# Kernel tuning notes

Measured on AMD Instinct MI355X. Metric: run time of the kernel, lower is better.

The kernel has to match this reference:

```python
import jax, jax.numpy as jnp
import numpy as np

B, T, INP, E, H, N = 16, 256, 1536, 512, 8, 16
D = E // H            # 64, must equal default dim_head for to_out shapes to work
SCALE = D ** -0.5
EPS = 1e-5


def _ln(x, g, b):
    m = x.mean(-1, keepdims=True)
    v = ((x - m) ** 2).mean(-1, keepdims=True)
    return (x - m) * jax.lax.rsqrt(v + EPS) * g + b


def _attend(q, k, v, Wo, bo):
    # q,k,v: [bt, h, n, d]. NOTE: attend is LogSoftmax, not Softmax (faithful).
    dots = jnp.einsum('bhnd,bhmd->bhnm', q, k) * SCALE
    a = jax.nn.log_softmax(dots, axis=-1)
    o = jnp.einsum('bhnm,bhmd->bhnd', a, v)
    o = o.transpose(0, 2, 1, 3).reshape(o.shape[0], N, E)  # b n (h d)
    return o @ Wo + bo


def _self_attn(x, Wqkv, Wo, bo):
    # x is already LayerNormed (PreNorm); residual adds the normed x (faithful).
    qkv = x @ Wqkv  # [bt, n, 3E]
    q, k, v = jnp.split(qkv, 3, axis=-1)
    hd = lambda t: t.reshape(t.shape[0], N, H, D).transpose(0, 2, 1, 3)
    return _attend(hd(q), hd(k), hd(v), Wo, bo) + x


def _ff(x, W1, b1, W2, b2):
    # x already LayerNormed; residual adds normed x (faithful to PreNorm+FF).
    return jax.nn.gelu(x @ W1 + b1, approximate=False) @ W2 + b2 + x


def setup_inputs() -> dict:
    key = jax.random.key(0)
    ks = iter(jax.random.split(key, 64))
    nrm = lambda shape, s=0.02: jax.random.normal(next(ks), shape, jnp.float32) * s
    inp = {
        'features': jax.random.normal(next(ks), (B, T, INP), jnp.float32),
        'targets_array': jax.random.randint(next(ks), (B, T), 0, N, jnp.int64),
        'emb': nrm((N, E), 1.0),
        'Wf': nrm((INP, 2 * E * N)), 'bf': jnp.zeros((2 * E * N,), jnp.float32),
        # layer 0: Attention (tuple path: only to_out used)
        'att0_Wo': nrm((E, E)), 'att0_bo': jnp.zeros((E,), jnp.float32),
        'Wm': nrm((E, 1)), 'bm': jnp.zeros((1,), jnp.float32),
    }
    for i in range(3):
        inp[f'ff{i}_g'] = jnp.ones((E,), jnp.float32)
        inp[f'ff{i}_b'] = jnp.zeros((E,), jnp.float32)
        inp[f'ff{i}_W1'] = nrm((E, 2 * E)); inp[f'ff{i}_b1'] = jnp.zeros((2 * E,), jnp.float32)
        inp[f'ff{i}_W2'] = nrm((2 * E, E)); inp[f'ff{i}_b2'] = jnp.zeros((E,), jnp.float32)
    for i in (1, 2):
        inp[f'att{i}_g'] = jnp.ones((E,), jnp.float32)
        inp[f'att{i}_b'] = jnp.zeros((E,), jnp.float32)
        inp[f'att{i}_Wqkv'] = nrm((E, 3 * E))
        inp[f'att{i}_Wo'] = nrm((E, E)); inp[f'att{i}_bo'] = jnp.zeros((E,), jnp.float32)
    return inp


def reference(features, targets_array, emb, Wf, bf, att0_Wo, att0_bo, Wm, bm,
              ff0_g, ff0_b, ff0_W1, ff0_b1, ff0_W2, ff0_b2,
              ff1_g, ff1_b, ff1_W1, ff1_b1, ff1_W2, ff1_b2,
              ff2_g, ff2_b, ff2_W1, ff2_b1, ff2_W2, ff2_b2,
              att1_g, att1_b, att1_Wqkv, att1_Wo, att1_bo,
              att2_g, att2_b, att2_Wqkv, att2_Wo, att2_bo):
    f = features.reshape(-1, INP)                 # [BT, INP]
    t = targets_array.reshape(-1)                 # [BT]
    kv = f @ Wf + bf                              # [BT, 2*E*N]
    k_, v_ = jnp.split(kv, 2, axis=-1)
    nhd = lambda x: x.reshape(-1, N, H, D).transpose(0, 2, 1, 3)  # b (n h d) -> b h n d
    k, v = nhd(k_), nhd(v_)
    q = emb[t].reshape(-1, H, 1, D)               # b h d -> b h 1 d
    q = jnp.broadcast_to(q, (q.shape[0], H, N, D))
    # layer stack: Attn(tuple), PreNorm(FF), PreNorm(Attn), PreNorm(FF), PreNorm(Attn), PreNorm(FF)
    x = _attend(q, k, v, att0_Wo, att0_bo)        # [BT, N, E]
    x = _ff(_ln(x, ff0_g, ff0_b), ff0_W1, ff0_b1, ff0_W2, ff0_b2)
    x = _self_attn(_ln(x, att1_g, att1_b), att1_Wqkv, att1_Wo, att1_bo)
    x = _ff(_ln(x, ff1_g, ff1_b), ff1_W1, ff1_b1, ff1_W2, ff1_b2)
    x = _self_attn(_ln(x, att2_g, att2_b), att2_Wqkv, att2_Wo, att2_bo)
    x = _ff(_ln(x, ff2_g, ff2_b), ff2_W1, ff2_b1, ff2_W2, ff2_b2)
    out = x.mean(axis=1)                          # mean over targets -> [BT, E]
    out = out.reshape(B, T, E)
    mean = out @ Wm + bm                          # [B, T, 1]
    return mean
```

## Files before the change

kernel.cpp:

```cpp
#include <hip/hip_runtime.h>
#include <math.h>

#define BTOT 4096
#define INP  1536
#define EDIM 512
#define NTOK 16
#define KVW  16384
#define ENW  8192
#define FFH  1024
#define NDOT 2048

typedef __attribute__((ext_vector_type(8))) __bf16 bf16x8;
typedef __attribute__((ext_vector_type(4))) float f32x4;

__device__ __forceinline__ ushort f2bf(float f) {
    union { float f; unsigned u; } v; v.f = f;
    unsigned r = v.u + 0x7fffu + ((v.u >> 16) & 1u);
    return (ushort)(r >> 16);
}
__device__ __forceinline__ float bf2f(ushort h) {
    union { unsigned u; float f; } v; v.u = ((unsigned)h) << 16;
    return v.f;
}

__device__ __forceinline__ void transpose_body(
    const float* in, int ld, int c0, int R, ushort* out,
    int bx, int by, int tid)
{
    __shared__ float t[64][65];
    const int bc = bx * 64 + c0;
    const int br = by * 64;
#pragma unroll
    for (int it = 0; it < 16; ++it) {
        int idx = tid + it * 256;
        int r = idx >> 6, c = idx & 63;
        t[r][c] = in[(size_t)(br + r) * ld + bc + c];
    }
    __syncthreads();
    const int C0 = bx * 64;
#pragma unroll
    for (int it = 0; it < 4; ++it) {
        int idx = tid + it * 256;
        int cc = idx >> 4, rp = idx & 15;
        uint2 w2;
        w2.x = f2bf(t[4 * rp + 0][cc]) | ((unsigned)f2bf(t[4 * rp + 1][cc]) << 16);
        w2.y = f2bf(t[4 * rp + 2][cc]) | ((unsigned)f2bf(t[4 * rp + 3][cc]) << 16);
        *reinterpret_cast<uint2*>(out + (size_t)(C0 + cc) * R + br + 4 * rp) = w2;
    }
}

struct TJob { const float* in; ushort* out; int ld, c0, R, gbx, boffs; };
struct TJobs { TJob j[10]; };

__global__ __launch_bounds__(256) void transpose_all_k(TJobs jobs)
{
    const int b = blockIdx.x;
    int ji = 0;
    while (ji < 9 && b >= jobs.j[ji + 1].boffs) ++ji;
    TJob jb = jobs.j[ji];
    const int rel = b - jb.boffs;
    transpose_body(jb.in, jb.ld, jb.c0, jb.R, jb.out,
                   rel % jb.gbx, rel / jb.gbx, threadIdx.x);
}

__global__ __launch_bounds__(256) void conv_all_k(
    const float* __restrict__ features, ushort* __restrict__ featb,
    const float* __restrict__ wq0, const float* __restrict__ wq1,
    ushort* __restrict__ wv0, ushort* __restrict__ wv1)
{
    const int b = blockIdx.x;
    if (b < 3072) {
        const int i = b * 256 + threadIdx.x;
        const float4* p = reinterpret_cast<const float4*>(features) + 2 * (size_t)i;
        float4 a = p[0], c = p[1];
        uint4 o;
        o.x = f2bf(a.x) | ((unsigned)f2bf(a.y) << 16);
        o.y = f2bf(a.z) | ((unsigned)f2bf(a.w) << 16);
        o.z = f2bf(c.x) | ((unsigned)f2bf(c.y) << 16);
        o.w = f2bf(c.z) | ((unsigned)f2bf(c.w) << 16);
        reinterpret_cast<uint4*>(featb)[i] = o;
    } else {
        const int bb = b - 3072;
        const float* src = (bb >= 128) ? wq1 : wq0;
        ushort* dst = (bb >= 128) ? wv1 : wv0;
        const int idx = (bb & 127) * 256 + threadIdx.x;
        const int row = idx >> 6, c8 = (idx & 63) * 8;
        const float4* p = reinterpret_cast<const float4*>(
            src + (size_t)row * (3 * EDIM) + 2 * EDIM + c8);
        float4 a = p[0], c = p[1];
        uint4 o;
        o.x = f2bf(a.x) | ((unsigned)f2bf(a.y) << 16);
        o.y = f2bf(a.z) | ((unsigned)f2bf(a.w) << 16);
        o.z = f2bf(c.x) | ((unsigned)f2bf(c.y) << 16);
        o.w = f2bf(c.z) | ((unsigned)f2bf(c.w) << 16);
        *reinterpret_cast<uint4*>(dst + (size_t)row * EDIM + c8) = o;
    }
}

__global__ __launch_bounds__(256) void gproj_k(
    const float* __restrict__ Wf, const float* __restrict__ bfv,
    const float* __restrict__ emb, ushort* __restrict__ BTg,
    float* __restrict__ C0s, const int* __restrict__ targets,
    int* __restrict__ perm, int* __restrict__ boff)
{
    if (blockIdx.y == 8) {
        if (blockIdx.x != 0) return;
        __shared__ int cnt[NTOK], off_s[NTOK], cur[NTOK];
        const int tid = threadIdx.x;
        if (tid < NTOK) cnt[tid] = 0;
        __syncthreads();
        for (int i = tid; i < BTOT; i += 256) atomicAdd(&cnt[targets[i]], 1);
        __syncthreads();
        if (tid == 0) {
            int s = 0;
            for (int b = 0; b < NTOK; ++b) { off_s[b] = s; cur[b] = s; s += cnt[b]; }
            for (int b = 0; b < NTOK; ++b) boff[b] = off_s[b];
            boff[NTOK] = s;
        }
        __syncthreads();
        for (int i = tid; i < BTOT; i += 256) {
            int t = targets[i];
            int p = atomicAdd(&cur[t], 1);
            perm[p] = i;
        }
        return;
    }

    const int hm = blockIdx.x;
    const int h = hm >> 4, m = hm & 15;
    const int l = threadIdx.x & 63, w = threadIdx.x >> 6;
    const int t = l & 15, isub = l >> 4;
    const int colb = m * 512 + h * 64;
    const int ibase = blockIdx.y * (INP / 8);

    float4 e[16];
#pragma unroll
    for (int q = 0; q < 16; ++q)
        e[q] = *reinterpret_cast<const float4*>(emb + t * EDIM + h * 64 + q * 4);

    const int n = t * 128 + hm;
    for (int i0 = ibase; i0 < ibase + INP / 8; i0 += 16) {
        const int i = i0 + w * 4 + isub;
        const float* wr = Wf + (size_t)i * KVW + colb;
        float acc = 0.f;
#pragma unroll
        for (int q = 0; q < 16; ++q) {
            float4 v4 = *reinterpret_cast<const float4*>(wr + q * 4);
            acc = fmaf(v4.x, e[q].x, fmaf(v4.y, e[q].y,
                  fmaf(v4.z, e[q].z, fmaf(v4.w, e[q].w, acc))));
        }
        BTg[(size_t)n * INP + i] = f2bf(acc);
    }
    if (blockIdx.y == 0 && w == 0 && isub == 0) {
        const float* br = bfv + colb;
        float acc = 0.f;
#pragma unroll
        for (int q = 0; q < 16; ++q) {
            float4 v4 = *reinterpret_cast<const float4*>(br + q * 4);
            acc = fmaf(v4.x, e[q].x, fmaf(v4.y, e[q].y,
                  fmaf(v4.z, e[q].z, fmaf(v4.w, e[q].w, acc))));
        }
        C0s[n] = 0.125f * acc;
    }
}

template <int BM, int BN, int WM, int WN, int NW, bool GELU, bool OUTBF>
__global__ __launch_bounds__(NW * 64) void gemm_mfma_k(
    const ushort* __restrict__ A, int lda,
    const ushort* __restrict__ BT, int ldb,
    void* __restrict__ Cp, int ldc, int K,
    const float* __restrict__ bias,
    const ushort* __restrict__ res, int ldr,
    float scale)
{
    static_assert((BM / WM) * (BN / WN) == NW, "wave grid");
    static_assert(BM % (NW * 8) == 0 && BN % (NW * 8) == 0, "staging");
    constexpr int FM = WM / 16, FN = WN / 16;
    constexpr int IA = BM * 8 / (NW * 64), IB = BN * 8 / (NW * 64);
    constexpr int RA = BM / NW, RB = BN / NW;

    __shared__ bf16x8 As[BM][8];
    __shared__ bf16x8 Bs[BN][8];
    const int tid = threadIdx.x;
    const int l   = tid & 63;
    const int w   = tid >> 6;
    const int wm  = w / (BN / WN), wn = w % (BN / WN);
    const int brow = blockIdx.y * BM, bcol = blockIdx.x * BN;

    const int lr = l >> 3;
    const int ls = (l & 7) ^ lr;
    const ushort* Ab = A  + (size_t)(brow + w * RA + lr) * lda + ls * 8;
    const ushort* Bb = BT + (size_t)(bcol + w * RB + lr) * ldb + ls * 8;

    f32x4 acc[FM][FN];
#pragma unroll
    for (int i = 0; i < FM; ++i)
#pragma unroll
        for (int j = 0; j < FN; ++j) acc[i][j] = (f32x4)0.f;

    for (int k0 = 0; k0 < K; k0 += 64) {
#pragma unroll
        for (int i = 0; i < IA; ++i)
            __builtin_amdgcn_global_load_lds(
                (const __attribute__((address_space(1))) void*)(Ab + (size_t)(i * 8) * lda + k0),
                (__attribute__((address_space(3))) void*)&As[w * RA + i * 8][0],
                16, 0, 0);
#pragma unroll
        for (int i = 0; i < IB; ++i)
            __builtin_amdgcn_global_load_lds(
                (const __attribute__((address_space(1))) void*)(Bb + (size_t)(i * 8) * ldb + k0),
                (__attribute__((address_space(3))) void*)&Bs[w * RB + i * 8][0],
                16, 0, 0);
        __syncthreads();
#pragma unroll
        for (int kh = 0; kh < 2; ++kh) {
            const int slot = (kh * 4 + (l >> 4)) ^ (l & 7);
            bf16x8 af[FM], bfr[FN];
#pragma unroll
            for (int mt = 0; mt < FM; ++mt)
                af[mt] = As[wm * WM + mt * 16 + (l & 15)][slot];
#pragma unroll
            for (int nt = 0; nt < FN; ++nt)
                bfr[nt] = Bs[wn * WN + nt * 16 + (l & 15)][slot];
#pragma unroll
            for (int mt = 0; mt < FM; ++mt)
#pragma unroll
                for (int nt = 0; nt < FN; ++nt)
                    acc[mt][nt] = __builtin_amdgcn_mfma_f32_16x16x32_bf16(
                        af[mt], bfr[nt], acc[mt][nt], 0, 0, 0);
        }
        __syncthreads();
    }

    const int cr = (l >> 4) * 4, cc = l & 15;
#pragma unroll
    for (int mt = 0; mt < FM; ++mt) {
#pragma unroll
        for (int nt = 0; nt < FN; ++nt) {
            const int gc = bcol + wn * WN + nt * 16 + cc;
            const float bv = bias ? bias[gc] : 0.f;
#pragma unroll
            for (int r = 0; r < 4; ++r) {
                const size_t gr = (size_t)brow + wm * WM + mt * 16 + cr + r;
                float v = acc[mt][nt][r] * scale + bv;
                if (GELU) v = 0.5f * v * (1.f + erff(v * 0.70710678118654752f));
                if (res) v += bf2f(res[gr * ldr + gc]);
                if (OUTBF) ((ushort*)Cp)[gr * ldc + gc] = f2bf(v);
                else       ((float*)Cp)[gr * ldc + gc]  = v;
            }
        }
    }
}

template <bool GELU, bool OUTBF>
__global__ __launch_bounds__(256, 3) void gemm_pipe64_k(
    const ushort* __restrict__ A, int lda,
    const ushort* __restrict__ BT, int ldb,
    void* __restrict__ Cp, int ldc, int K,
    const float* __restrict__ bias,
    const ushort* __restrict__ res, int ldr,
    float scale)
{
    __shared__ bf16x8 Asl[2][64][8];
    __shared__ bf16x8 Bsl[2][128][8];
    const int tid = threadIdx.x;
    const int l = tid & 63, w = tid >> 6;
    const int wm = w >> 1, wn = w & 1;
    const int brow = blockIdx.y * 64, bcol = blockIdx.x * 128;
    const int lr = l >> 3, ls = (l & 7) ^ lr;

    const ushort* Ab = A  + (size_t)(brow + w * 16 + lr) * lda + ls * 8;
    const ushort* Bb = BT + (size_t)(bcol + w * 32 + lr) * ldb + ls * 8;

#define STAGE_P(d, t) do { const int k0s = (t) * 64;                          \
    _Pragma("unroll")                                                          \
    for (int g = 0; g < 2; ++g)                                                \
        __builtin_amdgcn_global_load_lds(                                      \
            (const __attribute__((address_space(1))) void*)(Ab + (size_t)(g * 8) * lda + k0s), \
            (__attribute__((address_space(3))) void*)&Asl[d][w * 16 + g * 8][0], 16, 0, 0);    \
    _Pragma("unroll")                                                          \
    for (int g = 0; g < 4; ++g)                                                \
        __builtin_amdgcn_global_load_lds(                                      \
            (const __attribute__((address_space(1))) void*)(Bb + (size_t)(g * 8) * ldb + k0s), \
            (__attribute__((address_space(3))) void*)&Bsl[d][w * 32 + g * 8][0], 16, 0, 0);    \
} while (0)

#define RD_AP(dst, dd, kh) do {                                                \
    const int slot_ = ((kh) * 4 + (l >> 4)) ^ (l & 7);                         \
    _Pragma("unroll")                                                          \
    for (int mt = 0; mt < 2; ++mt)                                             \
        dst[mt] = Asl[dd][wm * 32 + mt * 16 + (l & 15)][slot_];                \
} while (0)

#define RD_BP(dd, kh) do {                                                     \
    const int slot_ = ((kh) * 4 + (l >> 4)) ^ (l & 7);                         \
    _Pragma("unroll")                                                          \
    for (int nt = 0; nt < 4; ++nt)                                             \
        bfr[nt][kh] = Bsl[dd][wn * 64 + nt * 16 + (l & 15)][slot_];            \
} while (0)

#define MFMA_P(af, kh) do {                                                    \
    __builtin_amdgcn_s_setprio(1);                                             \
    _Pragma("unroll")                                                          \
    for (int mt = 0; mt < 2; ++mt)                                             \
        _Pragma("unroll")                                                      \
        for (int nt = 0; nt < 4; ++nt)                                         \
            acc[mt][nt] = __builtin_amdgcn_mfma_f32_16x16x32_bf16(             \
                af[mt], bfr[nt][kh], acc[mt][nt], 0, 0, 0);                    \
    __builtin_amdgcn_s_setprio(0);                                             \
} while (0)

    f32x4 acc[2][4];
#pragma unroll
    for (int i = 0; i < 2; ++i)
#pragma unroll
        for (int j = 0; j < 4; ++j) acc[i][j] = (f32x4)0.f;

    STAGE_P(0, 0);
    STAGE_P(1, 1);
    asm volatile("s_waitcnt vmcnt(6)" ::: "memory");
    __builtin_amdgcn_s_barrier();

    bf16x8 aA[2], aB[2], bfr[4][2];
    RD_AP(aA, 0, 0);
    RD_BP(0, 0);

    const int NT = K / 64;
    for (int j = 0; j < NT; ++j) {
        const int d = j & 1;
        if (j > 0 && j + 1 < NT) STAGE_P(d ^ 1, j + 1);
        RD_AP(aB, d, 1);
        RD_BP(d, 1);
        MFMA_P(aA, 0);
        MFMA_P(aB, 1);
        __syncthreads();
        if (j + 1 < NT) {
            RD_AP(aA, d ^ 1, 0);
            RD_BP(d ^ 1, 0);
        }
    }
#undef STAGE_P
#undef RD_AP
#undef RD_BP
#undef MFMA_P

    const int cr = (l >> 4) * 4, cc = l & 15;
#pragma unroll
    for (int mt = 0; mt < 2; ++mt) {
#pragma unroll
        for (int nt = 0; nt < 4; ++nt) {
            const int gc = bcol + wn * 64 + nt * 16 + cc;
            const float bv = bias ? bias[gc] : 0.f;
#pragma unroll
            for (int r = 0; r < 4; ++r) {
                const size_t gr = (size_t)brow + wm * 32 + mt * 16 + cr + r;
                float v = acc[mt][nt][r] * scale + bv;
                if (GELU) v = 0.5f * v * (1.f + erff(v * 0.70710678118654752f));
                if (res) v += bf2f(res[gr * ldr + gc]);
                if (OUTBF) ((ushort*)Cp)[gr * ldc + gc] = f2bf(v);
                else       ((float*)Cp)[gr * ldc + gc]  = v;
            }
        }
    }
}

__global__ __launch_bounds__(512, 2) void gemm_v256_k(
    const ushort* __restrict__ A,
    const ushort* __restrict__ BT,
    const float* __restrict__ bias,
    ushort* __restrict__ C)
{
    __shared__ bf16x8 lds[2][2][256][8];
    const int tid = threadIdx.x;
    const int l = tid & 63, w = tid >> 6;
    const int wm = w >> 2, wn = w & 3;
    const int brow = blockIdx.y * 256, bcol = blockIdx.x * 256;
    const int lr = l >> 3, ls = (l & 7) ^ lr;

    const ushort* Ab = A  + (size_t)(brow + w * 8 + lr) * INP + ls * 8;
    const ushort* Bb = BT + (size_t)(bcol + w * 8 + lr) * INP + ls * 8;

#define STAGE_T(d, t) do { const int k0s = (t) * 64;                          \
    _Pragma("unroll")                                                          \
    for (int g = 0; g < 4; ++g)                                                \
        __builtin_amdgcn_global_load_lds(                                      \
            (const __attribute__((address_space(1))) void*)(Ab + (size_t)(g * 64) * INP + k0s), \
            (__attribute__((address_space(3))) void*)&lds[d][0][g * 64 + w * 8][0], 16, 0, 0);  \
    _Pragma("unroll")                                                          \
    for (int g = 0; g < 4; ++g)                                                \
        __builtin_amdgcn_global_load_lds(                                      \
            (const __attribute__((address_space(1))) void*)(Bb + (size_t)(g * 64) * INP + k0s), \
            (__attribute__((address_space(3))) void*)&lds[d][1][g * 64 + w * 8][0], 16, 0, 0);  \
} while (0)

#define RD_A(dst, dd, rh, kh) do {                                             \
    const int slot_ = ((kh) * 4 + (l >> 4)) ^ (l & 7);                         \
    _Pragma("unroll")                                                          \
    for (int mt = 0; mt < 4; ++mt)                                             \
        dst[mt] = lds[dd][0][wm * 128 + (rh) * 64 + mt * 16 + (l & 15)][slot_]; \
} while (0)

#define RD_B(dd, kh) do {                                                      \
    const int slot_ = ((kh) * 4 + (l >> 4)) ^ (l & 7);                         \
    _Pragma("unroll")                                                          \
    for (int nt = 0; nt < 4; ++nt)                                             \
        bfr[nt][kh] = lds[dd][1][wn * 64 + nt * 16 + (l & 15)][slot_];         \
} while (0)

#define MFMA4(base, af, kh) do {                                               \
    __builtin_amdgcn_s_setprio(1);                                             \
    _Pragma("unroll")                                                          \
    for (int mt = 0; mt < 4; ++mt)                                             \
        _Pragma("unroll")                                                      \
        for (int nt = 0; nt < 4; ++nt)                                         \
            acc[(base) + mt][nt] = __builtin_amdgcn_mfma_f32_16x16x32_bf16(    \
                af[mt], bfr[nt][kh], acc[(base) + mt][nt], 0, 0, 0);           \
    __builtin_amdgcn_s_setprio(0);                                             \
} while (0)

    f32x4 acc[8][4];
#pragma unroll
    for (int i = 0; i < 8; ++i)
#pragma unroll
        for (int j = 0; j < 4; ++j) acc[i][j] = (f32x4)0.f;

    STAGE_T(0, 0);
    STAGE_T(1, 1);
    asm volatile("s_waitcnt vmcnt(8)" ::: "memory");
    __builtin_amdgcn_s_barrier();

    bf16x8 aA[4], aB[4], bfr[4][2];
    RD_A(aA, 0, 0, 0);
    RD_B(0, 0);

    const int NT = INP / 64;
    for (int j = 0; j < NT; ++j) {
        const int d = j & 1;
        if (j > 0 && j + 1 < NT) STAGE_T(d ^ 1, j + 1);
        RD_A(aB, d, 0, 1);
        RD_B(d, 1);
        MFMA4(0, aA, 0);
        RD_A(aA, d, 1, 0);
        MFMA4(0, aB, 1);
        RD_A(aB, d, 1, 1);
        MFMA4(4, aA, 0);
        MFMA4(4, aB, 1);
        __syncthreads();
        if (j + 1 < NT) {
            RD_A(aA, d ^ 1, 0, 0);
            RD_B(d ^ 1, 0);
        }
    }
#undef STAGE_T
#undef RD_A
#undef RD_B
#undef MFMA4

    const int cr = (l >> 4) * 4, cc = l & 15;
#pragma unroll
    for (int h = 0; h < 2; ++h)
#pragma unroll
        for (int mt = 0; mt < 4; ++mt)
#pragma unroll
            for (int nt = 0; nt < 4; ++nt) {
                const int gc = bcol + wn * 64 + nt * 16 + cc;
                const float bv = bias[gc];
#pragma unroll
                for (int r = 0; r < 4; ++r) {
                    const size_t gr = (size_t)brow + wm * 128 + h * 64 + mt * 16 + cr + r;
                    C[gr * ENW + gc] = f2bf(acc[h * 4 + mt][nt][r] + bv);
                }
            }
}

__global__ __launch_bounds__(256) void gemm_dots_k(
    const ushort* __restrict__ A,
    const ushort* __restrict__ BT,
    const int* __restrict__ perm, const int* __restrict__ boff,
    const float* __restrict__ C0s, float* __restrict__ Csel)
{
    const int bucket = blockIdx.y;
    const int off = boff[bucket], end = boff[bucket + 1];
    const int tile = blockIdx.x;
    if (tile * 128 >= end - off) return;

    __shared__ bf16x8 As[128][8];
    __shared__ bf16x8 Bs[128][8];
    const int tid = threadIdx.x;
    const int l = tid & 63, w = tid >> 6;
    const int wm = w >> 1, wn = w & 1;
    const int lr = l >> 3;
    const int ls = (l & 7) ^ lr;

    int rowidx[4];
#pragma unroll
    for (int i = 0; i < 4; ++i) {
        int rg = off + tile * 128 + w * 32 + lr + i * 8;
        rowidx[i] = perm[rg < end ? rg : off];
    }
    const ushort* Bb = BT + (size_t)(bucket * 128 + w * 32 + lr) * INP + ls * 8;

    f32x4 acc[4][4];
#pragma unroll
    for (int i = 0; i < 4; ++i)
#pragma unroll
        for (int j = 0; j < 4; ++j) acc[i][j] = (f32x4)0.f;

    for (int k0 = 0; k0 < INP; k0 += 64) {
#pragma unroll
        for (int i = 0; i < 4; ++i)
            __builtin_amdgcn_global_load_lds(
                (const __attribute__((address_space(1))) void*)(
                    A + (size_t)rowidx[i] * INP + ls * 8 + k0),
                (__attribute__((address_space(3))) void*)&As[w * 32 + i * 8][0],
                16, 0, 0);
#pragma unroll
        for (int i = 0; i < 4; ++i)
            __builtin_amdgcn_global_load_lds(
                (const __attribute__((address_space(1))) void*)(
                    Bb + (size_t)(i * 8) * INP + k0),
                (__attribute__((address_space(3))) void*)&Bs[w * 32 + i * 8][0],
                16, 0, 0);
        __syncthreads();
#pragma unroll
        for (int kh = 0; kh < 2; ++kh) {
            const int slot = (kh * 4 + (l >> 4)) ^ (l & 7);
            bf16x8 af[4], bfr[4];
#pragma unroll
            for (int mt = 0; mt < 4; ++mt)
                af[mt] = As[wm * 64 + mt * 16 + (l & 15)][slot];
#pragma unroll
            for (int nt = 0; nt < 4; ++nt)
                bfr[nt] = Bs[wn * 64 + nt * 16 + (l & 15)][slot];
#pragma unroll
            for (int mt = 0; mt < 4; ++mt)
#pragma unroll
                for (int nt = 0; nt < 4; ++nt)
                    acc[mt][nt] = __builtin_amdgcn_mfma_f32_16x16x32_bf16(
                        af[mt], bfr[nt], acc[mt][nt], 0, 0, 0);
        }
        __syncthreads();
    }

    const int cr = (l >> 4) * 4, cc = l & 15;
#pragma unroll
    for (int mt = 0; mt < 4; ++mt) {
#pragma unroll
        for (int nt = 0; nt < 4; ++nt) {
            const int gc = wn * 64 + nt * 16 + cc;
            const float bv = C0s[bucket * 128 + gc];
#pragma unroll
            for (int r = 0; r < 4; ++r) {
                float val = acc[mt][nt][r] * 0.125f + bv;
                float mx = val;
                mx = fmaxf(mx, __shfl_xor(mx, 1, 64));
                mx = fmaxf(mx, __shfl_xor(mx, 2, 64));
                mx = fmaxf(mx, __shfl_xor(mx, 4, 64));
                mx = fmaxf(mx, __shfl_xor(mx, 8, 64));
                float e = expf(val - mx);
                e += __shfl_xor(e, 1, 64);
                e += __shfl_xor(e, 2, 64);
                e += __shfl_xor(e, 4, 64);
                e += __shfl_xor(e, 8, 64);
                const float lse = mx + logf(e);
                int rg = off + tile * 128 + wm * 64 + mt * 16 + cr + r;
                int orow = perm[rg < end ? rg : off];
                Csel[(size_t)orow * 128 + gc] = val - lse;
            }
        }
    }
}

__global__ __launch_bounds__(512) void attend0_k(
    const float* __restrict__ dsel, const ushort* __restrict__ vb,
    ushort* __restrict__ o)
{
    const int bt = blockIdx.x;
    const int l  = threadIdx.x & 63;
    const int h  = threadIdx.x >> 6;
    const int dg = l & 7, mg = l >> 3;

    const float w0 = dsel[(size_t)bt * 128 + h * 16 + mg];
    const float w1 = dsel[(size_t)bt * 128 + h * 16 + 8 + mg];

    const ushort* base = vb + (size_t)bt * ENW + h * 64 + dg * 8;
    uint4 v0 = *reinterpret_cast<const uint4*>(base + (size_t)mg * EDIM);
    uint4 v1 = *reinterpret_cast<const uint4*>(base + (size_t)(8 + mg) * EDIM);
    const ushort* u0 = reinterpret_cast<const ushort*>(&v0);
    const ushort* u1 = reinterpret_cast<const ushort*>(&v1);
    float acc[8];
#pragma unroll
    for (int j = 0; j < 8; ++j)
        acc[j] = w0 * bf2f(u0[j]) + w1 * bf2f(u1[j]);
#pragma unroll
    for (int off = 8; off < 64; off <<= 1)
#pragma unroll
        for (int j = 0; j < 8; ++j) acc[j] += __shfl_xor(acc[j], off, 64);

    if (mg == 0) {
        uint4 pk;
        pk.x = f2bf(acc[0]) | ((unsigned)f2bf(acc[1]) << 16);
        pk.y = f2bf(acc[2]) | ((unsigned)f2bf(acc[3]) << 16);
        pk.z = f2bf(acc[4]) | ((unsigned)f2bf(acc[5]) << 16);
        pk.w = f2bf(acc[6]) | ((unsigned)f2bf(acc[7]) << 16);
        *reinterpret_cast<uint4*>(o + (size_t)bt * EDIM + h * 64 + dg * 8) = pk;
    }
}

__global__ __launch_bounds__(256) void ln_k(
    const float* __restrict__ x, const float* __restrict__ g,
    const float* __restrict__ b, ushort* __restrict__ yb)
{
    const int row = blockIdx.x * 4 + (threadIdx.x >> 6);
    const int lane = threadIdx.x & 63;
    const float* xr = x + (size_t)row * EDIM + lane * 8;
    float4 a0 = *reinterpret_cast<const float4*>(xr);
    float4 a1 = *reinterpret_cast<const float4*>(xr + 4);
    float v[8] = {a0.x, a0.y, a0.z, a0.w, a1.x, a1.y, a1.z, a1.w};

    float s = 0.f;
#pragma unroll
    for (int j = 0; j < 8; ++j) s += v[j];
#pragma unroll
    for (int off = 32; off; off >>= 1) s += __shfl_xor(s, off, 64);
    const float m = s * (1.f / 512.f);

    float q = 0.f;
#pragma unroll
    for (int j = 0; j < 8; ++j) { float d = v[j] - m; q = fmaf(d, d, q); }
#pragma unroll
    for (int off = 32; off; off >>= 1) q += __shfl_xor(q, off, 64);
    const float inv = rsqrtf(q * (1.f / 512.f) + 1e-5f);

    const int c = lane * 8;
    float4 g0 = *reinterpret_cast<const float4*>(g + c);
    float4 g1 = *reinterpret_cast<const float4*>(g + c + 4);
    float4 b0 = *reinterpret_cast<const float4*>(b + c);
    float4 b1 = *reinterpret_cast<const float4*>(b + c + 4);
    float gg[8] = {g0.x, g0.y, g0.z, g0.w, g1.x, g1.y, g1.z, g1.w};
    float bb[8] = {b0.x, b0.y, b0.z, b0.w, b1.x, b1.y, b1.z, b1.w};
    float out[8];
#pragma unroll
    for (int j = 0; j < 8; ++j) out[j] = (v[j] - m) * inv * gg[j] + bb[j];
    uint4 p;
    p.x = f2bf(out[0]) | ((unsigned)f2bf(out[1]) << 16);
    p.y = f2bf(out[2]) | ((unsigned)f2bf(out[3]) << 16);
    p.z = f2bf(out[4]) | ((unsigned)f2bf(out[5]) << 16);
    p.w = f2bf(out[6]) | ((unsigned)f2bf(out[7]) << 16);
    *reinterpret_cast<uint4*>(yb + (size_t)row * EDIM + c) = p;
}

__global__ __launch_bounds__(256) void final_k(
    const float* __restrict__ x, const float* __restrict__ Wm,
    const float* __restrict__ bm, float* __restrict__ out)
{
    const int row = blockIdx.x * 4 + (threadIdx.x >> 6);
    const int lane = threadIdx.x & 63;
    const float* xr = x + (size_t)row * EDIM + lane * 8;
    const float* wr = Wm + lane * 8;
    float s = 0.f;
#pragma unroll
    for (int j = 0; j < 8; ++j) s = fmaf(xr[j], wr[j], s);
#pragma unroll
    for (int off = 32; off; off >>= 1) s += __shfl_xor(s, off, 64);
    if (lane == 0) out[row] = s + bm[0];
}

extern "C" void kernel_launch(void* const* d_in, const int* in_sizes, int n_in,
                              void* d_out, int out_size, void* d_ws, size_t ws_size,
                              hipStream_t stream)
{
    (void)in_sizes; (void)n_in; (void)out_size; (void)ws_size;
    const float* features = (const float*)d_in[0];
    const int*   targets  = (const int*)d_in[1];
    const float* emb      = (const float*)d_in[2];
    const float* Wf       = (const float*)d_in[3];
    const float* bfv      = (const float*)d_in[4];
    const float* a0Wo     = (const float*)d_in[5];
    const float* a0bo     = (const float*)d_in[6];
    const float* Wm       = (const float*)d_in[7];
    const float* bm       = (const float*)d_in[8];
    const float *ffg[3], *ffb[3], *W1[3], *b1[3], *W2[3], *b2[3];
    for (int i = 0; i < 3; ++i) {
        ffg[i] = (const float*)d_in[9 + 6 * i];
        ffb[i] = (const float*)d_in[10 + 6 * i];
        W1[i]  = (const float*)d_in[11 + 6 * i];
        b1[i]  = (const float*)d_in[12 + 6 * i];
        W2[i]  = (const float*)d_in[13 + 6 * i];
        b2[i]  = (const float*)d_in[14 + 6 * i];
    }
    const float *ag[2], *abp[2], *aWqkv[2], *aWo[2], *abo[2];
    for (int i = 0; i < 2; ++i) {
        ag[i]    = (const float*)d_in[27 + 5 * i];
        abp[i]   = (const float*)d_in[28 + 5 * i];
        aWqkv[i] = (const float*)d_in[29 + 5 * i];
        aWo[i]   = (const float*)d_in[30 + 5 * i];
        abo[i]   = (const float*)d_in[31 + 5 * i];
    }

    char* wsc = (char*)d_ws;
    auto alloc = [&](size_t bytes) { char* p = wsc; wsc += bytes; return p; };
    ushort* WfvT  = (ushort*)alloc((size_t)ENW * INP * 2);
    ushort* BTg   = (ushort*)alloc((size_t)NDOT * INP * 2);
    float*  C0s   = (float*) alloc((size_t)NDOT * 4);
    float*  dsel  = (float*) alloc((size_t)BTOT * 128 * 4);
    int*    perm  = (int*)   alloc((size_t)BTOT * 4);
    int*    boff  = (int*)   alloc(32 * 4);
    ushort* a0WoT = (ushort*)alloc((size_t)EDIM * EDIM * 2);
    ushort *W1T[3], *W2T[3], *WoT[2], *Wv_bf[2], *WcombT[2];
    for (int i = 0; i < 3; ++i) {
        W1T[i] = (ushort*)alloc((size_t)FFH * EDIM * 2);
        W2T[i] = (ushort*)alloc((size_t)EDIM * FFH * 2);
    }
    for (int i = 0; i < 2; ++i) {
        WoT[i]    = (ushort*)alloc((size_t)EDIM * EDIM * 2);
        Wv_bf[i]  = (ushort*)alloc((size_t)EDIM * EDIM * 2);
        WcombT[i] = (ushort*)alloc((size_t)EDIM * EDIM * 2);
    }
    ushort* featb = (ushort*)alloc((size_t)BTOT * INP * 2);
    ushort* o_b   = (ushort*)alloc((size_t)BTOT * EDIM * 2);
    float*  x     = (float*) alloc((size_t)BTOT * EDIM * 4);
    ushort* xlnb  = (ushort*)alloc((size_t)BTOT * EDIM * 2);
    ushort* hb    = (ushort*)alloc((size_t)BTOT * FFH * 2);
    ushort* vb    = (ushort*)alloc((size_t)BTOT * ENW * 2);

    const dim3 blk(256, 1, 1);

    conv_all_k<<<3328, blk, 0, stream>>>(features, featb,
                                         aWqkv[0], aWqkv[1], Wv_bf[0], Wv_bf[1]);
    gproj_k<<<dim3(128, 9), blk, 0, stream>>>(Wf, bfv, emb, BTg, C0s,
                                              targets, perm, boff);

    TJobs tj;
    int ob = 0, ji = 0;
    auto addj = [&](const float* in, ushort* out, int ld, int c0, int R,
                    int gbx, int gby) {
        tj.j[ji++] = {in, out, ld, c0, R, gbx, ob};
        ob += gbx * gby;
    };
    addj(Wf, WfvT, KVW, ENW, INP, 128, 24);
    addj(a0Wo, a0WoT, EDIM, 0, EDIM, 8, 8);
    for (int i = 0; i < 3; ++i) {
        addj(W1[i], W1T[i], FFH, 0, EDIM, 16, 8);
        addj(W2[i], W2T[i], EDIM, 0, FFH, 8, 16);
    }
    addj(aWo[0], WoT[0], EDIM, 0, EDIM, 8, 8);
    addj(aWo[1], WoT[1], EDIM, 0, EDIM, 8, 8);
    transpose_all_k<<<ob, blk, 0, stream>>>(tj);

    const float CATT = -44.36141955583650f;
    gemm_dots_k<<<dim3(32, 16), blk, 0, stream>>>(featb, BTg, perm, boff,
                                                  C0s, dsel);
    for (int i = 0; i < 2; ++i)
        gemm_mfma_k<64, 128, 32, 64, 4, false, true>
            <<<dim3(EDIM / 128, EDIM / 64), blk, 0, stream>>>(
            WoT[i], EDIM, Wv_bf[i], EDIM, WcombT[i], EDIM, EDIM,
            nullptr, nullptr, 0, CATT);
    gemm_v256_k<<<dim3(ENW / 256, BTOT / 256), dim3(512, 1, 1), 0, stream>>>(
        featb, WfvT, bfv + ENW, vb);
    attend0_k<<<BTOT, 512, 0, stream>>>(dsel, vb, o_b);
    gemm_pipe64_k<false, false>
        <<<dim3(EDIM / 128, BTOT / 64), blk, 0, stream>>>(
        o_b, EDIM, a0WoT, EDIM, x, EDIM, EDIM, a0bo, nullptr, 0, 1.f);

    auto ln = [&](const float* g, const float* b) {
        ln_k<<<BTOT / 4, blk, 0, stream>>>(x, g, b, xlnb);
    };
    auto ff = [&](int i) {
        ln(ffg[i], ffb[i]);
        gemm_pipe64_k<true, true>
            <<<dim3(FFH / 128, BTOT / 64), blk, 0, stream>>>(
            xlnb, EDIM, W1T[i], EDIM, hb, FFH, EDIM, b1[i], nullptr, 0, 1.f);
        gemm_pipe64_k<false, false>
            <<<dim3(EDIM / 128, BTOT / 64), blk, 0, stream>>>(
            hb, FFH, W2T[i], FFH, x, EDIM, FFH, b2[i], xlnb, EDIM, 1.f);
    };
    auto attn = [&](int i) {
        ln(ag[i], abp[i]);
        gemm_pipe64_k<false, false>
            <<<dim3(EDIM / 128, BTOT / 64), blk, 0, stream>>>(
            xlnb, EDIM, WcombT[i], EDIM, x, EDIM, EDIM, abo[i], xlnb, EDIM, 1.f);
    };

    ff(0);
    attn(0);
    ff(1);
    attn(1);
    ff(2);

    final_k<<<BTOT / 4, blk, 0, stream>>>(x, Wm, bm, (float*)d_out);
}
```

Baseline: 413.4 us.

## Double-buffer the gathered dots GEMM with prefetch and reuse pipelined GEMM

```diff
diff --git a/kernel.cpp b/kernel.cpp
--- a/kernel.cpp
+++ b/kernel.cpp
@@ -164,94 +164,6 @@
     }
 }
 
-template <int BM, int BN, int WM, int WN, int NW, bool GELU, bool OUTBF>
-__global__ __launch_bounds__(NW * 64) void gemm_mfma_k(
-    const ushort* __restrict__ A, int lda,
-    const ushort* __restrict__ BT, int ldb,
-    void* __restrict__ Cp, int ldc, int K,
-    const float* __restrict__ bias,
-    const ushort* __restrict__ res, int ldr,
-    float scale)
-{
-    static_assert((BM / WM) * (BN / WN) == NW, "wave grid");
-    static_assert(BM % (NW * 8) == 0 && BN % (NW * 8) == 0, "staging");
-    constexpr int FM = WM / 16, FN = WN / 16;
-    constexpr int IA = BM * 8 / (NW * 64), IB = BN * 8 / (NW * 64);
-    constexpr int RA = BM / NW, RB = BN / NW;
-
-    __shared__ bf16x8 As[BM][8];
-    __shared__ bf16x8 Bs[BN][8];
-    const int tid = threadIdx.x;
-    const int l   = tid & 63;
-    const int w   = tid >> 6;
-    const int wm  = w / (BN / WN), wn = w % (BN / WN);
-    const int brow = blockIdx.y * BM, bcol = blockIdx.x * BN;
-
-    const int lr = l >> 3;
-    const int ls = (l & 7) ^ lr;
-    const ushort* Ab = A  + (size_t)(brow + w * RA + lr) * lda + ls * 8;
-    const ushort* Bb = BT + (size_t)(bcol + w * RB + lr) * ldb + ls * 8;
-
-    f32x4 acc[FM][FN];
-#pragma unroll
-    for (int i = 0; i < FM; ++i)
-#pragma unroll
-        for (int j = 0; j < FN; ++j) acc[i][j] = (f32x4)0.f;
-
-    for (int k0 = 0; k0 < K; k0 += 64) {
-#pragma unroll
-        for (int i = 0; i < IA; ++i)
-            __builtin_amdgcn_global_load_lds(
-                (const __attribute__((address_space(1))) void*)(Ab + (size_t)(i * 8) * lda + k0),
-                (__attribute__((address_space(3))) void*)&As[w * RA + i * 8][0],
-                16, 0, 0);
-#pragma unroll
-        for (int i = 0; i < IB; ++i)
-            __builtin_amdgcn_global_load_lds(
-                (const __attribute__((address_space(1))) void*)(Bb + (size_t)(i * 8) * ldb + k0),
-                (__attribute__((address_space(3))) void*)&Bs[w * RB + i * 8][0],
-                16, 0, 0);
-        __syncthreads();
-#pragma unroll
-        for (int kh = 0; kh < 2; ++kh) {
-            const int slot = (kh * 4 + (l >> 4)) ^ (l & 7);
-            bf16x8 af[FM], bfr[FN];
-#pragma unroll
-            for (int mt = 0; mt < FM; ++mt)
-                af[mt] = As[wm * WM + mt * 16 + (l & 15)][slot];
-#pragma unroll
-            for (int nt = 0; nt < FN; ++nt)
-                bfr[nt] = Bs[wn * WN + nt * 16 + (l & 15)][slot];
-#pragma unroll
-            for (int mt = 0; mt < FM; ++mt)
-#pragma unroll
-                for (int nt = 0; nt < FN; ++nt)
-                    acc[mt][nt] = __builtin_amdgcn_mfma_f32_16x16x32_bf16(
-                        af[mt], bfr[nt], acc[mt][nt], 0, 0, 0);
-        }
-        __syncthreads();
-    }
-
-    const int cr = (l >> 4) * 4, cc = l & 15;
-#pragma unroll
-    for (int mt = 0; mt < FM; ++mt) {
-#pragma unroll
-        for (int nt = 0; nt < FN; ++nt) {
-            const int gc = bcol + wn * WN + nt * 16 + cc;
-            const float bv = bias ? bias[gc] : 0.f;
-#pragma unroll
-            for (int r = 0; r < 4; ++r) {
-                const size_t gr = (size_t)brow + wm * WM + mt * 16 + cr + r;
-                float v = acc[mt][nt][r] * scale + bv;
-                if (GELU) v = 0.5f * v * (1.f + erff(v * 0.70710678118654752f));
-                if (res) v += bf2f(res[gr * ldr + gc]);
-                if (OUTBF) ((ushort*)Cp)[gr * ldc + gc] = f2bf(v);
-                else       ((float*)Cp)[gr * ldc + gc]  = v;
-            }
-        }
-    }
-}
-
 template <bool GELU, bool OUTBF>
 __global__ __launch_bounds__(256, 3) void gemm_pipe64_k(
     const ushort* __restrict__ A, int lda,
@@ -473,7 +385,7 @@
             }
 }
 
-__global__ __launch_bounds__(256) void gemm_dots_k(
+__global__ __launch_bounds__(256, 2) void gemm_dots_k(
     const ushort* __restrict__ A,
     const ushort* __restrict__ BT,
     const int* __restrict__ perm, const int* __restrict__ boff,
@@ -484,63 +396,93 @@
     const int tile = blockIdx.x;
     if (tile * 128 >= end - off) return;
 
-    __shared__ bf16x8 As[128][8];
-    __shared__ bf16x8 Bs[128][8];
+    __shared__ bf16x8 Asl[2][128][8];
+    __shared__ bf16x8 Bsl[2][128][8];
     const int tid = threadIdx.x;
     const int l = tid & 63, w = tid >> 6;
     const int wm = w >> 1, wn = w & 1;
     const int lr = l >> 3;
     const int ls = (l & 7) ^ lr;
 
-    int rowidx[4];
+    const ushort* Asrc[4];
 #pragma unroll
     for (int i = 0; i < 4; ++i) {
         int rg = off + tile * 128 + w * 32 + lr + i * 8;
-        rowidx[i] = perm[rg < end ? rg : off];
+        Asrc[i] = A + (size_t)perm[rg < end ? rg : off] * INP + ls * 8;
     }
     const ushort* Bb = BT + (size_t)(bucket * 128 + w * 32 + lr) * INP + ls * 8;
 
+#define DSTAGE(d, t) do { const int k0s = (t) * 64;                           \
+    _Pragma("unroll")                                                          \
+    for (int g = 0; g < 4; ++g)                                                \
+        __builtin_amdgcn_global_load_lds(                                      \
+            (const __attribute__((address_space(1))) void*)(Asrc[g] + k0s),    \
+            (__attribute__((address_space(3))) void*)&Asl[d][w * 32 + g * 8][0], 16, 0, 0);    \
+    _Pragma("unroll")                                                          \
+    for (int g = 0; g < 4; ++g)                                                \
+        __builtin_amdgcn_global_load_lds(                                      \
+            (const __attribute__((address_space(1))) void*)(Bb + (size_t)(g * 8) * INP + k0s), \
+            (__attribute__((address_space(3))) void*)&Bsl[d][w * 32 + g * 8][0], 16, 0, 0);    \
+} while (0)
+
+#define DRD_A(dst, dd, kh) do {                                                \
+    const int slot_ = ((kh) * 4 + (l >> 4)) ^ (l & 7);                         \
+    _Pragma("unroll")                                                          \
+    for (int mt = 0; mt < 4; ++mt)                                             \
+        dst[mt] = Asl[dd][wm * 64 + mt * 16 + (l & 15)][slot_];                \
+} while (0)
+
+#define DRD_B(dd, kh) do {                                                     \
+    const int slot_ = ((kh) * 4 + (l >> 4)) ^ (l & 7);                         \
+    _Pragma("unroll")                                                          \
+    for (int nt = 0; nt < 4; ++nt)                                             \
+        bfr[nt][kh] = Bsl[dd][wn * 64 + nt * 16 + (l & 15)][slot_];            \
+} while (0)
+
+#define DMFMA(af, kh) do {                                                     \
+    __builtin_amdgcn_s_setprio(1);                                             \
+    _Pragma("unroll")                                                          \
+    for (int mt = 0; mt < 4; ++mt)                                             \
+        _Pragma("unroll")                                                      \
+        for (int nt = 0; nt < 4; ++nt)                                         \
+            acc[mt][nt] = __builtin_amdgcn_mfma_f32_16x16x32_bf16(             \
+                af[mt], bfr[nt][kh], acc[mt][nt], 0, 0, 0);                    \
+    __builtin_amdgcn_s_setprio(0);                                             \
+} while (0)
+
     f32x4 acc[4][4];
 #pragma unroll
     for (int i = 0; i < 4; ++i)
 #pragma unroll
         for (int j = 0; j < 4; ++j) acc[i][j] = (f32x4)0.f;
 
-    for (int k0 = 0; k0 < INP; k0 += 64) {
-#pragma unroll
-        for (int i = 0; i < 4; ++i)
-            __builtin_amdgcn_global_load_lds(
-                (const __attribute__((address_space(1))) void*)(
-                    A + (size_t)rowidx[i] * INP + ls * 8 + k0),
-                (__attribute__((address_space(3))) void*)&As[w * 32 + i * 8][0],
-                16, 0, 0);
-#pragma unroll
-        for (int i = 0; i < 4; ++i)
-            __builtin_amdgcn_global_load_lds(
-                (const __attribute__((address_space(1))) void*)(
-                    Bb + (size_t)(i * 8) * INP + k0),
-                (__attribute__((address_space(3))) void*)&Bs[w * 32 + i * 8][0],
-                16, 0, 0);
+    DSTAGE(0, 0);
+    DSTAGE(1, 1);
+    asm volatile("s_waitcnt vmcnt(8)" ::: "memory");
+    __builtin_amdgcn_s_barrier();
+
+    bf16x8 aA[4], aB[4], bfr[4][2];
+    DRD_A(aA, 0, 0);
+    DRD_B(0, 0);
+
+    const int NT = INP / 64;
+    for (int j = 0; j < NT; ++j) {
+        const int d = j & 1;
+        if (j > 0 && j + 1 < NT) DSTAGE(d ^ 1, j + 1);
+        DRD_A(aB, d, 1);
+        DRD_B(d, 1);
+        DMFMA(aA, 0);
+        DMFMA(aB, 1);
         __syncthreads();
-#pragma unroll
-        for (int kh = 0; kh < 2; ++kh) {
-            const int slot = (kh * 4 + (l >> 4)) ^ (l & 7);
-            bf16x8 af[4], bfr[4];
-#pragma unroll
-            for (int mt = 0; mt < 4; ++mt)
-                af[mt] = As[wm * 64 + mt * 16 + (l & 15)][slot];
-#pragma unroll
-            for (int nt = 0; nt < 4; ++nt)
-                bfr[nt] = Bs[wn * 64 + nt * 16 + (l & 15)][slot];
-#pragma unroll
-            for (int mt = 0; mt < 4; ++mt)
-#pragma unroll
-                for (int nt = 0; nt < 4; ++nt)
-                    acc[mt][nt] = __builtin_amdgcn_mfma_f32_16x16x32_bf16(
-                        af[mt], bfr[nt], acc[mt][nt], 0, 0, 0);
-        }
-        __syncthreads();
-    }
+        if (j + 1 < NT) {
+            DRD_A(aA, d ^ 1, 0);
+            DRD_B(d ^ 1, 0);
+        }
+    }
+#undef DSTAGE
+#undef DRD_A
+#undef DRD_B
+#undef DMFMA
 
     const int cr = (l >> 4) * 4, cc = l & 15;
 #pragma unroll
@@ -752,7 +694,7 @@
     gemm_dots_k<<<dim3(32, 16), blk, 0, stream>>>(featb, BTg, perm, boff,
                                                   C0s, dsel);
     for (int i = 0; i < 2; ++i)
-        gemm_mfma_k<64, 128, 32, 64, 4, false, true>
+        gemm_pipe64_k<false, true>
             <<<dim3(EDIM / 128, EDIM / 64), blk, 0, stream>>>(
             WoT[i], EDIM, Wv_bf[i], EDIM, WcombT[i], EDIM, EDIM,
             nullptr, nullptr, 0, CATT);
```

New measurement: 404.8 us. 1.02x faster.
